# Optimization experiments

Hardware: AMD Instinct MI355X
Metric: run time of the kernel (lower is better)

## Reference

```python
import jax, jax.numpy as jnp
import numpy as np

# ---- geometry / physics constants (from setup_params) ----
H = 400; W_CROP = 400
PSF_W = 121          # interpolated_psf_width
CLEAR = 20           # clear_dist
_m = int(np.ceil(PSF_W / 2 - CLEAR + 2))
MARGIN = _m + _m % 2                    # 44
IM = H + 2 * MARGIN                     # 488
MAG = 100.0; PX_CCD = 11.0              # M, pixel_size_CCD
NZ = 64; Z_MIN = -2.0; Z_MAX = 2.0      # psf bank z sampling
SIGMA_READ = 10.0                       # read noise std (counts)
N_EMIT = 2048


def setup_inputs() -> dict:
    key = jax.random.key(0)
    k1, k2, k3, k4 = jax.random.split(key, 4)
    # emitter positions (um): xy in [-15,15] (stays inside canvas), z in [-2,2]
    lo = jnp.array([-15.0, -15.0, Z_MIN], jnp.float32)
    hi = jnp.array([15.0, 15.0, Z_MAX], jnp.float32)
    local_xyz = jax.random.uniform(k1, (1, N_EMIT, 3), jnp.float32) * (hi - lo) + lo
    Nphotons = jax.random.uniform(k2, (1, N_EMIT), jnp.float32) * 4000.0 + 1000.0
    xy_center = jnp.zeros((2,), jnp.float32)  # FOV center; unused when fd_flag=False
    psf_bank = jax.random.uniform(k3, (NZ, PSF_W, PSF_W), jnp.float32)  # positive PSFs
    noise_map = jax.random.normal(k4, (H, W_CROP), jnp.float32)         # unit gaussians
    return {"local_xyz": local_xyz, "Nphotons": Nphotons, "xy_center": xy_center,
            "psf_bank": psf_bank, "noise_map": noise_map}


def reference(local_xyz, Nphotons, xy_center, psf_bank, noise_map):
    x = local_xyz[0, :, 0]                       # [N] um
    y = local_xyz[0, :, 1]
    z = local_xyz[0, :, 2]
    nph = Nphotons[0]                            # [N]

    # psf_module(0,0,z): nearest-z lookup in precomputed bank (fd_flag=False)
    zi = jnp.clip(jnp.round((z - Z_MIN) / (Z_MAX - Z_MIN) * (NZ - 1)),
                  0, NZ - 1).astype(jnp.int32)
    psf = psf_bank[zi]                           # [N, PSF_W, PSF_W]

    # emitter position in camera pixels
    lx = x * MAG / PX_CCD
    ly = y * MAG / PX_CCD
    r0f = ly + IM / 2 - PSF_W / 2
    c0f = lx + IM / 2 - PSF_W / 2
    r0 = jnp.floor(r0f).astype(jnp.int32)        # [N] integer splat origin
    c0 = jnp.floor(c0f).astype(jnp.int32)
    rs = (r0f - jnp.floor(r0f))[:, None, None]   # sub-pixel shift in [0,1)
    cs = (c0f - jnp.floor(c0f))[:, None, None]

    # sub-pixel shift (bilinear, zero-fill boundary): out[i,j] = in[i-rs, j-cs]
    P = jnp.pad(psf, ((0, 0), (1, 0), (1, 0)))
    sh = ((1 - rs) * (1 - cs) * P[:, 1:, 1:] + rs * (1 - cs) * P[:, :-1, 1:]
          + (1 - rs) * cs * P[:, 1:, :-1] + rs * cs * P[:, :-1, :-1])
    sh = jnp.abs(sh)
    sh = sh / sh.sum(axis=(1, 2), keepdims=True) * nph[:, None, None]

    # scatter-add splat into shared canvas
    ar = jnp.arange(PSF_W, dtype=jnp.int32)
    rows = r0[:, None, None] + ar[None, :, None]  # [N, PSF_W, 1]
    cols = c0[:, None, None] + ar[None, None, :]  # [N, 1, PSF_W]
    canvas = jnp.zeros((IM, IM), sh.dtype).at[rows, cols].add(sh)

    im = canvas[MARGIN:MARGIN + H, MARGIN:MARGIN + W_CROP]

    # NoiseLayer: Gaussian approx of Poisson shot + read noise
    im_noisy = im + jnp.sqrt(jnp.maximum(im, 0.0) + SIGMA_READ ** 2) * noise_map

    # project_01 normalization
    return (im_noisy - im_noisy.min()) / (im_noisy.max() - im_noisy.min())
```

## Files before the change

kernel.cpp:

```cpp
#include <hip/hip_runtime.h>

#define H        400
#define W_CROP   400
#define PSF_W    121
#define MARGIN   44
#define IM       488
#define NZ       64
#define N_EMIT   2048
#define PSF_AREA (PSF_W * PSF_W)
#define SIGMA2   100.0f
#define TILE     16
#define TB       25
#define NTILES   (TB * TB)
#define NPIX     (H * W_CROP)
#define PADW     152
#define PADA     (PADW * PADW)
#define CHUNKS   4
#define CAPC     224
#define CAP_B    512
#define NBUCK    (TB * CHUNKS)
#define PADBLK   512

static __device__ __forceinline__ unsigned enc_ord(float f) {
    unsigned u = __float_as_uint(f);
    return (u & 0x80000000u) ? ~u : (u | 0x80000000u);
}
static __device__ __forceinline__ float dec_ord(unsigned u) {
    return __uint_as_float((u & 0x80000000u) ? (u & 0x7fffffffu) : ~u);
}

static __device__ __forceinline__ void geom_of(const float* __restrict__ xyz, int e,
                                               int& r0, int& c0, int& zi,
                                               float& r0f, float& c0f) {
    const float x = xyz[3 * e + 0];
    const float y = xyz[3 * e + 1];
    const float z = xyz[3 * e + 2];
    const float lx = (x * 100.0f) / 11.0f;
    const float ly = (y * 100.0f) / 11.0f;
    r0f = (ly + 244.0f) - 60.5f;
    c0f = (lx + 244.0f) - 60.5f;
    r0 = (int)floorf(r0f);
    c0 = (int)floorf(c0f);
    zi = (int)rintf((z + 2.0f) / 4.0f * 63.0f);
    zi = min(max(zi, 0), NZ - 1);
}

__global__ __launch_bounds__(256) void prep_kernel(
        const float* __restrict__ psf_bank, float* __restrict__ zpart,
        float* __restrict__ pad, unsigned* __restrict__ minmax,
        const float* __restrict__ xyz, const float* __restrict__ nph_arr,
        float4* __restrict__ bucket, int* __restrict__ bcnt)
{
    __shared__ float red[4][4];
    __shared__ int   wtot[4];

    if (blockIdx.x < PADBLK) {
        const int zi   = blockIdx.x >> 3;
        const int part = blockIdx.x & 7;

        if (blockIdx.x == 0 && threadIdx.x == 0) { minmax[0] = 0xFFFFFFFFu; minmax[1] = 0u; }

        const float* __restrict__ src = psf_bank + (size_t)zi * PSF_AREA;
        float* __restrict__ dst = pad + (size_t)zi * PADA;

        const int plo = part * 2888;
        const int phi = min(plo + 2888, PADA);
        for (int i = plo + (int)threadIdx.x; i < phi; i += 256) {
            const int rp = i / PADW;
            const int r = rp - 16;
            const int c = i - rp * PADW - 16;
            const bool in = ((unsigned)r < (unsigned)PSF_W) && ((unsigned)c < (unsigned)PSF_W);
            dst[i] = in ? src[r * PSF_W + c] : 0.0f;
        }

        const int slo = part * 1831;
        const int shi = min(slo + 1831, PSF_AREA);
        float S = 0.f, R = 0.f, C = 0.f, K = 0.f;
        for (int i = slo + (int)threadIdx.x; i < shi; i += 256) {
            const float v = src[i];
            const int r = i / PSF_W;
            const int c = i - r * PSF_W;
            S += v;
            if (r == PSF_W - 1) R += v;
            if (c == PSF_W - 1) C += v;
            if (r == PSF_W - 1 && c == PSF_W - 1) K += v;
        }
        #pragma unroll
        for (int off = 32; off > 0; off >>= 1) {
            S += __shfl_down(S, off, 64);
            R += __shfl_down(R, off, 64);
            C += __shfl_down(C, off, 64);
            K += __shfl_down(K, off, 64);
        }
        const int wave = threadIdx.x >> 6, lane = threadIdx.x & 63;
        if (lane == 0) { red[wave][0] = S; red[wave][1] = R; red[wave][2] = C; red[wave][3] = K; }
        __syncthreads();
        if (threadIdx.x == 0) {
            float4 o;
            o.x = (red[0][0] + red[1][0]) + (red[2][0] + red[3][0]);
            o.y = (red[0][1] + red[1][1]) + (red[2][1] + red[3][1]);
            o.z = (red[0][2] + red[1][2]) + (red[2][2] + red[3][2]);
            o.w = (red[0][3] + red[1][3]) + (red[2][3] + red[3][3]);
            *(float4*)(zpart + (size_t)(zi * 8 + part) * 4) = o;
        }
        return;
    }

    const int b   = blockIdx.x - PADBLK;
    const int btr = b >> 2, bzc = b & 3;
    const int w    = threadIdx.x >> 6;
    const int lane = threadIdx.x & 63;

    int mycnt = 0;
    unsigned mymask = 0u;
    #pragma unroll
    for (int q = 0; q < 8; ++q) {
        const int e = (int)threadIdx.x * 8 + q;
        int r0, c0, zi; float r0f, c0f;
        geom_of(xyz, e, r0, c0, zi, r0f, c0f);
        const bool p = ((zi >> 4) == bzc)
                     && (btr >= ((r0 - MARGIN) >> 4)) && (btr <= ((r0 + 76) >> 4));
        mymask |= (unsigned)p << q;
        mycnt += (int)p;
    }

    int incl = mycnt;
    #pragma unroll
    for (int off = 1; off < 64; off <<= 1) {
        const int v = __shfl_up(incl, off, 64);
        if (lane >= off) incl += v;
    }
    if (lane == 63) wtot[w] = incl;
    __syncthreads();
    int base = incl - mycnt;
    #pragma unroll
    for (int ww = 0; ww < 4; ++ww) base += (ww < w) ? wtot[ww] : 0;
    const int ntot = wtot[0] + wtot[1] + wtot[2] + wtot[3];

    if (mymask) {
        int slot = base;
        #pragma unroll
        for (int q = 0; q < 8; ++q) {
            if (mymask & (1u << q)) {
                const int e = (int)threadIdx.x * 8 + q;
                int r0, c0, zi; float r0f, c0f;
                geom_of(xyz, e, r0, c0, zi, r0f, c0f);
                if (slot < CAP_B) {
                    const float rs = r0f - floorf(r0f);
                    const float cs = c0f - floorf(c0f);
                    const float nph = nph_arr[e];
                    float4 s0, s1;
                    s0.x = nph * (1.0f - rs) * (1.0f - cs);
                    s0.y = nph * (1.0f - rs) * cs;
                    s0.z = nph * rs * (1.0f - cs);
                    s0.w = nph * rs * cs;
                    const int packed = ((r0 + 16) << 15) | ((c0 + 16) << 6) | zi;
                    s1.x = rs; s1.y = cs; s1.z = __int_as_float(packed); s1.w = 0.f;
                    bucket[(size_t)(b * CAP_B + slot) * 2]     = s0;
                    bucket[(size_t)(b * CAP_B + slot) * 2 + 1] = s1;
                }
                ++slot;
            }
        }
    }
    if (threadIdx.x == 0) bcnt[b] = min(ntot, CAP_B);
}

__global__ __launch_bounds__(256) void gather_kernel(
        const float* __restrict__ pad, const float4* __restrict__ bucket,
        const int* __restrict__ bcnt, const float* __restrict__ zpart,
        float* __restrict__ parts)
{
    const int zc   = (blockIdx.x & 7) >> 1;
    const int tile = 2 * (blockIdx.x >> 3) + (blockIdx.x & 1);
    if (tile >= NTILES) return;

    __shared__ float4 smeta[2 * CAPC];
    __shared__ float  tilepart[4][256];
    __shared__ int    wtot[4];

    const int tr = tile / TB, tc = tile - tr * TB;
    const int w    = threadIdx.x >> 6;
    const int lane = threadIdx.x & 63;
    const int px = lane & 15;
    const int wy = lane >> 4;
    const int orow0 = tr * TILE + wy * 4;
    const int ocol  = tc * TILE + px;
    const int crow0 = orow0 + MARGIN;
    const int ccol  = ocol + MARGIN;
    const int tcb   = (crow0 * PADW + ccol) * 4;
    const char* __restrict__ pbase = (const char*)pad;

    const int b   = tr * CHUNKS + zc;
    const int n_b = bcnt[b];
    const float4* __restrict__ bk = bucket + (size_t)b * CAP_B * 2;

    int nstaged = 0;
    for (int base_i = 0; base_i < n_b; base_i += 256) {
        const int i = base_i + (int)threadIdx.x;
        float4 m0, m1;
        int r0 = 0, c0 = 0, zi = 0;
        bool p = false;
        if (i < n_b) {
            m0 = bk[2 * i];
            m1 = bk[2 * i + 1];
            const int packed = __float_as_int(m1.z);
            zi = packed & 63;
            c0 = ((packed >> 6) & 511) - 16;
            r0 = ((packed >> 15) & 511) - 16;
            p = (tc >= ((c0 - MARGIN) >> 4)) && (tc <= ((c0 + 76) >> 4));
        }
        int incl = (int)p;
        #pragma unroll
        for (int off = 1; off < 64; off <<= 1) {
            const int v = __shfl_up(incl, off, 64);
            if (lane >= off) incl += v;
        }
        if (lane == 63) wtot[w] = incl;
        __syncthreads();
        int slot = nstaged + incl - (int)p;
        #pragma unroll
        for (int ww = 0; ww < 4; ++ww) slot += (ww < w) ? wtot[ww] : 0;
        const int round_tot = wtot[0] + wtot[1] + wtot[2] + wtot[3];
        if (p && slot < CAPC) {
            const float rs = m1.x, cs = m1.y;
            const float4* __restrict__ zp = (const float4*)zpart + zi * 8;
            float4 zm = zp[0];
            #pragma unroll
            for (int u = 1; u < 8; ++u) {
                const float4 t = zp[u];
                zm.x += t.x; zm.y += t.y; zm.z += t.z; zm.w += t.w;
            }
            const float ssum = zm.x - rs * zm.y - cs * zm.z + rs * cs * zm.w;
            const float inv = 1.0f / ssum;
            float4 s0, s1;
            s0.x = m0.x * inv; s0.y = m0.y * inv; s0.z = m0.z * inv; s0.w = m0.w * inv;
            const int offb = (zi * PADA + (15 - r0) * PADW + (16 - c0)) * 4;
            s1.x = __int_as_float(offb);
            s1.y = __int_as_float(r0);
            s1.z = __int_as_float(c0);
            s1.w = 0.f;
            smeta[2 * slot]     = s0;
            smeta[2 * slot + 1] = s1;
        }
        nstaged += round_tot;
        __syncthreads();
    }
    const int n = min(nstaged, CAPC);

    float acc0[4] = {0.f, 0.f, 0.f, 0.f};
    float acc1[4] = {0.f, 0.f, 0.f, 0.f};

    auto body = [&](int j, float* acc) {
        const float4 wt = smeta[2 * j];
        const float4 mm = smeta[2 * j + 1];
        const int off = __float_as_int(mm.x);
        const int pr0 = crow0 - __float_as_int(mm.y);
        const int pc  = ccol  - __float_as_int(mm.z);
        const char* __restrict__ p = pbase + (tcb + off);
        float a[5], b2[5];
        #pragma unroll
        for (int i = 0; i < 5; ++i) a[i] = *(const float*)(p + i * (PADW * 4));
        #pragma unroll
        for (int i = 0; i < 5; ++i) b2[i] = __shfl_up(a[i], 1, 16);
        if (px == 0) {
            #pragma unroll
            for (int i = 0; i < 5; ++i) b2[i] = *(const float*)(p - 4 + i * (PADW * 4));
        }
        const bool pcok = (unsigned)pc <= 120u;
        #pragma unroll
        for (int k = 0; k < 4; ++k) {
            float v = wt.x * a[k + 1];
            v = fmaf(wt.y, b2[k + 1], v);
            v = fmaf(wt.z, a[k],      v);
            v = fmaf(wt.w, b2[k],     v);
            const bool ok = pcok & ((unsigned)(pr0 + k) <= 120u);
            acc[k] += ok ? v : 0.f;
        }
    };

    int j = w;
    for (; j + 4 < n; j += 8) { body(j, acc0); body(j + 4, acc1); }
    if (j < n) body(j, acc0);

    #pragma unroll
    for (int k = 0; k < 4; ++k)
        tilepart[w][(wy * 4 + k) * 16 + px] = acc0[k] + acc1[k];
    __syncthreads();

    const int row = threadIdx.x >> 4, col = threadIdx.x & 15;
    const float s = ((tilepart[0][threadIdx.x] + tilepart[1][threadIdx.x]) +
                     (tilepart[2][threadIdx.x] + tilepart[3][threadIdx.x]));
    parts[(size_t)zc * NPIX + (tr * TILE + row) * W_CROP + (tc * TILE + col)] = s;
}

__global__ __launch_bounds__(256) void noise_minmax_kernel(
        const float* __restrict__ parts, const float* __restrict__ noise,
        float* __restrict__ out, unsigned* __restrict__ minmax)
{
    const int i = blockIdx.x * 256 + threadIdx.x;
    float vmin = 1e30f, vmax = -1e30f;
    if (i < NPIX / 4) {
        const float4 p0 = ((const float4*)parts)[i];
        const float4 p1 = ((const float4*)(parts + NPIX))[i];
        const float4 p2 = ((const float4*)(parts + 2 * NPIX))[i];
        const float4 p3 = ((const float4*)(parts + 3 * NPIX))[i];
        float4 im;
        im.x = (p0.x + p1.x) + (p2.x + p3.x);
        im.y = (p0.y + p1.y) + (p2.y + p3.y);
        im.z = (p0.z + p1.z) + (p2.z + p3.z);
        im.w = (p0.w + p1.w) + (p2.w + p3.w);
        const float4 nz = ((const float4*)noise)[i];
        im.x += sqrtf(fmaxf(im.x, 0.f) + SIGMA2) * nz.x;
        im.y += sqrtf(fmaxf(im.y, 0.f) + SIGMA2) * nz.y;
        im.z += sqrtf(fmaxf(im.z, 0.f) + SIGMA2) * nz.z;
        im.w += sqrtf(fmaxf(im.w, 0.f) + SIGMA2) * nz.w;
        ((float4*)out)[i] = im;
        vmin = fminf(fminf(im.x, im.y), fminf(im.z, im.w));
        vmax = fmaxf(fmaxf(im.x, im.y), fmaxf(im.z, im.w));
    }
    #pragma unroll
    for (int off = 32; off > 0; off >>= 1) {
        vmin = fminf(vmin, __shfl_down(vmin, off, 64));
        vmax = fmaxf(vmax, __shfl_down(vmax, off, 64));
    }
    if ((threadIdx.x & 63) == 0) {
        atomicMin(&minmax[0], enc_ord(vmin));
        atomicMax(&minmax[1], enc_ord(vmax));
    }
}

__global__ __launch_bounds__(256) void finalize_kernel(float* __restrict__ out,
                                                       const unsigned* __restrict__ minmax)
{
    const int i = blockIdx.x * 256 + threadIdx.x;
    if (i >= NPIX / 4) return;
    const float mn = dec_ord(minmax[0]);
    const float inv = 1.0f / (dec_ord(minmax[1]) - mn);
    float4 v = ((float4*)out)[i];
    v.x = (v.x - mn) * inv;
    v.y = (v.y - mn) * inv;
    v.z = (v.z - mn) * inv;
    v.w = (v.w - mn) * inv;
    ((float4*)out)[i] = v;
}

extern "C" void kernel_launch(void* const* d_in, const int* in_sizes, int n_in,
                              void* d_out, int out_size, void* d_ws, size_t ws_size,
                              hipStream_t stream) {
    const float* xyz      = (const float*)d_in[0];
    const float* nph      = (const float*)d_in[1];
    const float* psf_bank = (const float*)d_in[3];
    const float* noise    = (const float*)d_in[4];
    float* out = (float*)d_out;

    char* ws = (char*)d_ws;
    unsigned* minmax = (unsigned*)(ws + 0);
    float*    zpart  = (float*)(ws + 1024);
    float*    pad    = (float*)(ws + 9216);
    float4*   bucket = (float4*)(ws + 5923840);
    int*      bcnt   = (int*)(ws + 7562240);
    float*    parts  = (float*)(ws + 7563264);

    prep_kernel<<<PADBLK + NBUCK, 256, 0, stream>>>(psf_bank, zpart, pad, minmax,
                                                    xyz, nph, bucket, bcnt);
    gather_kernel<<<2504, 256, 0, stream>>>(pad, bucket, bcnt, zpart, parts);
    noise_minmax_kernel<<<(NPIX / 4 + 255) / 256, 256, 0, stream>>>(parts, noise, out, minmax);
    finalize_kernel<<<(NPIX / 4 + 255) / 256, 256, 0, stream>>>(out, minmax);
}
```

Before: 66.16 us.

## Store padded PSF bank as float2 pairs to drop shuffles and edge loads

```diff
diff --git a/kernel.cpp b/kernel.cpp
--- a/kernel.cpp
+++ b/kernel.cpp
@@ -47,7 +47,7 @@
 
 __global__ __launch_bounds__(256) void prep_kernel(
         const float* __restrict__ psf_bank, float* __restrict__ zpart,
-        float* __restrict__ pad, unsigned* __restrict__ minmax,
+        float2* __restrict__ pad2, unsigned* __restrict__ minmax,
         const float* __restrict__ xyz, const float* __restrict__ nph_arr,
         float4* __restrict__ bucket, int* __restrict__ bcnt)
 {
@@ -61,7 +61,7 @@
         if (blockIdx.x == 0 && threadIdx.x == 0) { minmax[0] = 0xFFFFFFFFu; minmax[1] = 0u; }
 
         const float* __restrict__ src = psf_bank + (size_t)zi * PSF_AREA;
-        float* __restrict__ dst = pad + (size_t)zi * PADA;
+        float2* __restrict__ dst = pad2 + (size_t)zi * PADA;
 
         const int plo = part * 2888;
         const int phi = min(plo + 2888, PADA);
@@ -69,8 +69,11 @@
             const int rp = i / PADW;
             const int r = rp - 16;
             const int c = i - rp * PADW - 16;
-            const bool in = ((unsigned)r < (unsigned)PSF_W) && ((unsigned)c < (unsigned)PSF_W);
-            dst[i] = in ? src[r * PSF_W + c] : 0.0f;
+            const bool rin = (unsigned)r < (unsigned)PSF_W;
+            float2 v;
+            v.x = (rin && (unsigned)(c - 1) < (unsigned)PSF_W) ? src[r * PSF_W + c - 1] : 0.0f;
+            v.y = (rin && (unsigned)c < (unsigned)PSF_W)       ? src[r * PSF_W + c]     : 0.0f;
+            dst[i] = v;
         }
 
         const int slo = part * 1831;
@@ -167,7 +170,7 @@
 }
 
 __global__ __launch_bounds__(256) void gather_kernel(
-        const float* __restrict__ pad, const float4* __restrict__ bucket,
+        const float2* __restrict__ pad2, const float4* __restrict__ bucket,
         const int* __restrict__ bcnt, const float* __restrict__ zpart,
         float* __restrict__ parts)
 {
@@ -188,8 +191,8 @@
     const int ocol  = tc * TILE + px;
     const int crow0 = orow0 + MARGIN;
     const int ccol  = ocol + MARGIN;
-    const int tcb   = (crow0 * PADW + ccol) * 4;
-    const char* __restrict__ pbase = (const char*)pad;
+    const int tcb2  = (crow0 * PADW + ccol) * 8;
+    const char* __restrict__ pbase = (const char*)pad2;
 
     const int b   = tr * CHUNKS + zc;
     const int n_b = bcnt[b];
@@ -235,7 +238,7 @@
             const float inv = 1.0f / ssum;
             float4 s0, s1;
             s0.x = m0.x * inv; s0.y = m0.y * inv; s0.z = m0.z * inv; s0.w = m0.w * inv;
-            const int offb = (zi * PADA + (15 - r0) * PADW + (16 - c0)) * 4;
+            const int offb = (zi * PADA + (15 - r0) * PADW + (16 - c0)) * 8;
             s1.x = __int_as_float(offb);
             s1.y = __int_as_float(r0);
             s1.z = __int_as_float(c0);
@@ -250,6 +253,8 @@
 
     float acc0[4] = {0.f, 0.f, 0.f, 0.f};
     float acc1[4] = {0.f, 0.f, 0.f, 0.f};
+    float acc2[4] = {0.f, 0.f, 0.f, 0.f};
+    float acc3[4] = {0.f, 0.f, 0.f, 0.f};
 
     auto body = [&](int j, float* acc) {
         const float4 wt = smeta[2 * j];
@@ -257,35 +262,31 @@
         const int off = __float_as_int(mm.x);
         const int pr0 = crow0 - __float_as_int(mm.y);
         const int pc  = ccol  - __float_as_int(mm.z);
-        const char* __restrict__ p = pbase + (tcb + off);
-        float a[5], b2[5];
-        #pragma unroll
-        for (int i = 0; i < 5; ++i) a[i] = *(const float*)(p + i * (PADW * 4));
-        #pragma unroll
-        for (int i = 0; i < 5; ++i) b2[i] = __shfl_up(a[i], 1, 16);
-        if (px == 0) {
-            #pragma unroll
-            for (int i = 0; i < 5; ++i) b2[i] = *(const float*)(p - 4 + i * (PADW * 4));
-        }
+        const char* __restrict__ p = pbase + (tcb2 + off);
+        float2 f[5];
+        #pragma unroll
+        for (int i = 0; i < 5; ++i) f[i] = *(const float2*)(p + i * (PADW * 8));
         const bool pcok = (unsigned)pc <= 120u;
         #pragma unroll
         for (int k = 0; k < 4; ++k) {
-            float v = wt.x * a[k + 1];
-            v = fmaf(wt.y, b2[k + 1], v);
-            v = fmaf(wt.z, a[k],      v);
-            v = fmaf(wt.w, b2[k],     v);
+            float v = wt.x * f[k + 1].y;
+            v = fmaf(wt.y, f[k + 1].x, v);
+            v = fmaf(wt.z, f[k].y,     v);
+            v = fmaf(wt.w, f[k].x,     v);
             const bool ok = pcok & ((unsigned)(pr0 + k) <= 120u);
             acc[k] += ok ? v : 0.f;
         }
     };
 
     int j = w;
-    for (; j + 4 < n; j += 8) { body(j, acc0); body(j + 4, acc1); }
-    if (j < n) body(j, acc0);
+    for (; j + 12 < n; j += 16) {
+        body(j, acc0); body(j + 4, acc1); body(j + 8, acc2); body(j + 12, acc3);
+    }
+    for (; j < n; j += 4) body(j, acc0);
 
     #pragma unroll
     for (int k = 0; k < 4; ++k)
-        tilepart[w][(wy * 4 + k) * 16 + px] = acc0[k] + acc1[k];
+        tilepart[w][(wy * 4 + k) * 16 + px] = (acc0[k] + acc1[k]) + (acc2[k] + acc3[k]);
     __syncthreads();
 
     const int row = threadIdx.x >> 4, col = threadIdx.x & 15;
@@ -357,14 +358,14 @@
     char* ws = (char*)d_ws;
     unsigned* minmax = (unsigned*)(ws + 0);
     float*    zpart  = (float*)(ws + 1024);
-    float*    pad    = (float*)(ws + 9216);
-    float4*   bucket = (float4*)(ws + 5923840);
-    int*      bcnt   = (int*)(ws + 7562240);
-    float*    parts  = (float*)(ws + 7563264);
-
-    prep_kernel<<<PADBLK + NBUCK, 256, 0, stream>>>(psf_bank, zpart, pad, minmax,
+    float2*   pad2   = (float2*)(ws + 9216);
+    float4*   bucket = (float4*)(ws + 11838464);
+    int*      bcnt   = (int*)(ws + 13476864);
+    float*    parts  = (float*)(ws + 13477888);
+
+    prep_kernel<<<PADBLK + NBUCK, 256, 0, stream>>>(psf_bank, zpart, pad2, minmax,
                                                     xyz, nph, bucket, bcnt);
-    gather_kernel<<<2504, 256, 0, stream>>>(pad, bucket, bcnt, zpart, parts);
+    gather_kernel<<<2504, 256, 0, stream>>>(pad2, bucket, bcnt, zpart, parts);
     noise_minmax_kernel<<<(NPIX / 4 + 255) / 256, 256, 0, stream>>>(parts, noise, out, minmax);
     finalize_kernel<<<(NPIX / 4 + 255) / 256, 256, 0, stream>>>(out, minmax);
 }
```

New measurement: 71.17 us. +7.6%, slower.
